# Kernel optimization log

Hardware: AMD Instinct MI355X
Metric: run time of the kernel (lower is better)

Reference implementation:

```python
import jax, jax.numpy as jnp
from jax import lax
import numpy as np

EPS = 1e-5
SCALE, K_UP = 2, 5  # CARAFE defaults


def conv(x, w, pad=0):
    return lax.conv_general_dilated(x, w, (1, 1), [(pad, pad), (pad, pad)],
                                    dimension_numbers=('NCHW', 'OIHW', 'NCHW'))


def bn(x, g, b, m, v):
    # eval-mode BatchNorm2d
    inv = g * lax.rsqrt(v + EPS)
    return x * inv[None, :, None, None] + (b - m * inv)[None, :, None, None]


def carafe(X, comp_w, comp_g, comp_bt, comp_m, comp_v, enc_w, enc_g, enc_bt, enc_m, enc_v):
    b, c, h, w = X.shape
    k2 = K_UP * K_UP
    W = jax.nn.relu(bn(conv(X, comp_w), comp_g, comp_bt, comp_m, comp_v))  # (b, c_mid, h, w)
    W = bn(conv(W, enc_w, pad=1), enc_g, enc_bt, enc_m, enc_v)             # (b, k2*SCALE^2, h, w)
    # PixelShuffle(SCALE): (b, k2*r^2, h, w) -> (b, k2, h*r, w*r)
    W = W.reshape(b, k2, SCALE, SCALE, h, w).transpose(0, 1, 4, 2, 5, 3)
    W = W.reshape(b, k2, h * SCALE, w * SCALE)
    W = jax.nn.softmax(W, axis=1)
    # nearest upsample by SCALE
    Xu = jnp.repeat(jnp.repeat(X, SCALE, axis=2), SCALE, axis=3)
    pad = (K_UP // 2) * SCALE
    Xp = jnp.pad(Xu, ((0, 0), (0, 0), (pad, pad), (pad, pad)))
    h_, w_ = h * SCALE, w * SCALE
    # Unfold(kernel=K_UP, dilation=SCALE): channel-major then kernel index, matching torch
    patches = jnp.stack([Xp[:, :, i * SCALE:i * SCALE + h_, j * SCALE:j * SCALE + w_]
                         for i in range(K_UP) for j in range(K_UP)], axis=2)  # (b,c,k2,h_,w_)
    return jnp.einsum('bkhw,bckhw->bchw', W, patches)


def setup_inputs():
    key = jax.random.key(0)
    ks = iter(jax.random.split(key, 80))
    nk = lambda: next(ks)
    P = lambda shape, s=0.05: jax.random.normal(nk(), shape, jnp.float32) * s
    d = {}
    B, C_out = 4, 64
    cins = [128, 256, 512]
    hw = [(96, 160), (48, 80), (24, 40)]
    for i, (ci, (h, w)) in enumerate(zip(cins, hw)):
        d[f'x{i}'] = jax.random.normal(nk(), (B, ci, h, w), jnp.float32)
        d[f'lat{i}_w'] = P((C_out, ci, 1, 1))
        d[f'lat{i}_b'] = P((C_out,))
        d[f'fpn{i}_w'] = P((C_out, C_out, 3, 3))
        d[f'fpn{i}_b'] = P((C_out,))
    k2s2 = (SCALE * K_UP) ** 2
    for u in range(2):
        d[f'u{u}_comp_w'] = P((C_out, C_out, 1, 1))
        d[f'u{u}_enc_w'] = P((k2s2, C_out, 3, 3))
        for nm, c in [('comp', C_out), ('enc', k2s2)]:
            d[f'u{u}_{nm}_g'] = 1.0 + P((c,))
            d[f'u{u}_{nm}_bt'] = P((c,))
            d[f'u{u}_{nm}_m'] = P((c,))
            d[f'u{u}_{nm}_v'] = jax.random.uniform(nk(), (c,), jnp.float32, 0.5, 1.5)
    return d


def reference(x0, x1, x2,
              lat0_w, lat0_b, fpn0_w, fpn0_b,
              lat1_w, lat1_b, fpn1_w, fpn1_b,
              lat2_w, lat2_b, fpn2_w, fpn2_b,
              u0_comp_w, u0_enc_w, u0_comp_g, u0_comp_bt, u0_comp_m, u0_comp_v,
              u0_enc_g, u0_enc_bt, u0_enc_m, u0_enc_v,
              u1_comp_w, u1_enc_w, u1_comp_g, u1_comp_bt, u1_comp_m, u1_comp_v,
              u1_enc_g, u1_enc_bt, u1_enc_m, u1_enc_v):
    lat = [conv(x, w) + b[None, :, None, None] for x, w, b in
           [(x0, lat0_w, lat0_b), (x1, lat1_w, lat1_b), (x2, lat2_w, lat2_b)]]
    # top-down pathway with CARAFE upsampling
    lat[1] = lat[1] + carafe(lat[2], u1_comp_w, u1_comp_g, u1_comp_bt, u1_comp_m, u1_comp_v,
                             u1_enc_w, u1_enc_g, u1_enc_bt, u1_enc_m, u1_enc_v)
    lat[0] = lat[0] + carafe(lat[1], u0_comp_w, u0_comp_g, u0_comp_bt, u0_comp_m, u0_comp_v,
                             u0_enc_w, u0_enc_g, u0_enc_bt, u0_enc_m, u0_enc_v)
    outs = tuple(conv(l, w, pad=1) + b[None, :, None, None] for l, w, b in
                 [(lat[0], fpn0_w, fpn0_b), (lat[1], fpn1_w, fpn1_b), (lat[2], fpn2_w, fpn2_b)])
    return outs
```

## Files before the change

### kernel.cpp

```cpp
#include <hip/hip_runtime.h>

#define BN_EPS 1e-5f

typedef __attribute__((ext_vector_type(8))) short bf16x8;
typedef __attribute__((ext_vector_type(4))) float f32x4;

__device__ __forceinline__ unsigned short f2bf(float f) {
    unsigned u = __float_as_uint(f);
    return (unsigned short)((u + 0x7fffu + ((u >> 16) & 1u)) >> 16);
}
__device__ __forceinline__ unsigned packbf(float lo, float hi) {
    return ((unsigned)f2bf(hi) << 16) | (unsigned)f2bf(lo);
}
__device__ __forceinline__ float bf2f(unsigned short u) {
    return __uint_as_float((unsigned)u << 16);
}
__device__ __forceinline__ bf16x8 ldw8(const float* p) {
    float4 a = *(const float4*)p;
    float4 b = *(const float4*)(p + 4);
    union { unsigned u[4]; bf16x8 v; } r;
    r.u[0] = packbf(a.x, a.y);
    r.u[1] = packbf(a.z, a.w);
    r.u[2] = packbf(b.x, b.y);
    r.u[3] = packbf(b.z, b.w);
    return r.v;
}

template<int COP, int CSPLIT, int MODE, bool OBF16>
__device__ __forceinline__
void conv3x3_body(int rem, int TX, unsigned short* xs,
                  const unsigned* __restrict__ xp,
                  const unsigned short* __restrict__ wt,
                  const float* __restrict__ p0, const float* __restrict__ p1,
                  const float* __restrict__ p2, const float* __restrict__ p3,
                  float* __restrict__ out, unsigned short* __restrict__ out_us,
                  int H, int W, int C_out)
{
    constexpr int NP = 324;
    constexpr int CT = COP / 16;
    static_assert(CT == CSPLIT, "CPB must be 1 (R1/R2 VGPR cliff)");

    int cs = rem % CSPLIT;
    int b  = (rem / CSPLIT) & 3;
    int t  = rem / (CSPLIT * 4);
    int x0 = (t % TX) * 16, y0 = (t / TX) * 16;

    int tid  = threadIdx.x;
    int lane = tid & 63, wid = tid >> 6;
    int lrow = lane >> 4, lcol = lane & 15;
    int HWp = H * W;

    int co0 = cs * 16;
    bool colok = (x0 + lcol) < W;

    f32x4 accA[2], accB[2];
#pragma unroll
    for (int rr = 0; rr < 2; ++rr) {
        accA[rr] = (f32x4){0.f, 0.f, 0.f, 0.f};
        accB[rr] = (f32x4){0.f, 0.f, 0.f, 0.f};
    }

    unsigned int* wsl = (unsigned int*)xs;

#pragma unroll 1
    for (int kb = 0; kb < 2; ++kb) {
        if (kb) __syncthreads();
        for (int p = tid; p < NP; p += 256) {
            int py = p / 18, px = p - py * 18;
            int gy = y0 + py - 1, gx = x0 + px - 1;
            bool ok = (gy >= 0) && (gy < H) && (gx >= 0) && (gx < W);
            const unsigned* gpp = xp + ((size_t)b * 32 + kb * 16) * HWp
                                     + (size_t)gy * W + gx;
#pragma unroll 8
            for (int cp = 0; cp < 16; ++cp) {
                unsigned pk = ok ? gpp[(size_t)cp * HWp] : 0u;
                wsl[((cp >> 2) * NP + p) * 4 + (cp & 3)] = pk;
            }
        }
        __syncthreads();

        bf16x8 a[9];
        const unsigned short* wl = wt + ((size_t)co0 + lcol) * 64 + kb * 32 + lrow * 8;
#pragma unroll
        for (int t9 = 0; t9 < 9; ++t9)
            a[t9] = *(const bf16x8*)(wl + (size_t)t9 * COP * 64);

#pragma unroll
        for (int rr = 0; rr < 2; ++rr) {
            int r0 = wid + rr * 8;
#pragma unroll
            for (int t9 = 0; t9 < 9; ++t9) {
                int dy = t9 / 3, dx = t9 - dy * 3;
                int g0 = lrow * NP + (r0 + dy) * 18 + lcol + dx;
                bf16x8 b0 = *(const bf16x8*)(xs + (size_t)g0 * 8);
                accA[rr] = __builtin_amdgcn_mfma_f32_16x16x32_bf16(a[t9], b0, accA[rr], 0, 0, 0);
                bf16x8 b1 = *(const bf16x8*)(xs + ((size_t)g0 + 4 * 18) * 8);
                accB[rr] = __builtin_amdgcn_mfma_f32_16x16x32_bf16(a[t9], b1, accB[rr], 0, 0, 0);
            }
        }
    }

    float sc[4], sh[4];
#pragma unroll
    for (int rg = 0; rg < 4; ++rg) {
        int co = co0 + lrow * 4 + rg;
        int cc = (co < C_out) ? co : 0;
        if (MODE == 0) { sc[rg] = 1.f; sh[rg] = p0[cc]; }
        else {
            float inv = p0[cc] * rsqrtf(p3[cc] + BN_EPS);
            sc[rg] = inv; sh[rg] = p1[cc] - p2[cc] * inv;
        }
    }
#pragma unroll
    for (int rr = 0; rr < 2; ++rr) {
        int r0 = wid + rr * 8;
        int yA = y0 + r0, yB = y0 + r0 + 4;
#pragma unroll
        for (int rg = 0; rg < 4; ++rg) {
            int co = co0 + lrow * 4 + rg;
            if (colok && co < C_out) {
                float vA = accA[rr][rg] * sc[rg] + sh[rg];
                float vB = accB[rr][rg] * sc[rg] + sh[rg];
                if (OBF16) {
                    unsigned short* oc = out_us + (((size_t)b * C_out + co) * H) * W + x0 + lcol;
                    if (yA < H) oc[(size_t)yA * W] = f2bf(vA);
                    if (yB < H) oc[(size_t)yB * W] = f2bf(vB);
                } else {
                    float* oc = out + (((size_t)b * C_out + co) * H) * W + x0 + lcol;
                    if (yA < H) oc[(size_t)yA * W] = vA;
                    if (yB < H) oc[(size_t)yB * W] = vB;
                }
            }
        }
    }
}

__global__ __launch_bounds__(256, 6)
void enc_fpn(int encBlocks,
             const unsigned* __restrict__ cxp, const unsigned short* __restrict__ wt_e,
             const float* __restrict__ g, const float* __restrict__ bt,
             const float* __restrict__ m, const float* __restrict__ v,
             unsigned short* __restrict__ enc_us, int He, int We, int TXe,
             const unsigned* __restrict__ xp, const unsigned short* __restrict__ wt_f,
             const float* __restrict__ bias, float* __restrict__ fout,
             int Hf, int Wf, int TXf)
{
    __shared__ unsigned short xs[4 * 324 * 8];
    int f = blockIdx.x;
    if (f < encBlocks)
        conv3x3_body<112, 7, 1, true>(f, TXe, xs, cxp, wt_e,
                                      g, bt, m, v, nullptr, enc_us, He, We, 100);
    else
        conv3x3_body<64, 4, 0, false>(f - encBlocks, TXf, xs, xp, wt_f,
                                      bias, nullptr, nullptr, nullptr, fout, nullptr, Hf, Wf, 64);
}

__global__ __launch_bounds__(256, 6)
void fpn_multi(const unsigned* __restrict__ l0p, const unsigned short* __restrict__ wt0,
               const float* __restrict__ b0, float* __restrict__ o0)
{
    __shared__ unsigned short xs[4 * 324 * 8];
    conv3x3_body<64, 4, 0, false>(blockIdx.x, 10, xs, l0p, wt0,
                                  b0, nullptr, nullptr, nullptr, o0, nullptr, 96, 160, 64);
}

template<int C_IN, int NPX, int MODE, bool INPK>
__device__ __forceinline__
void conv1x1_body(int f, unsigned short* xs,
                  const float* __restrict__ x, const unsigned* __restrict__ xp,
                  const float* __restrict__ wf,
                  const float* __restrict__ p0, const float* __restrict__ p1,
                  const float* __restrict__ p2, const float* __restrict__ p3,
                  unsigned* __restrict__ outp, int HW)
{
    constexpr int NT = NPX / 16;
    constexpr int QUADS = NPX / 4;
    int nb = HW / NPX;
    int px0 = (f % nb) * NPX;
    int b   = f / nb;

    int tid = threadIdx.x;
    int lane = tid & 63, wid = tid >> 6;
    int lrow = lane >> 4, lcol = lane & 15;
    const float*    xb  = INPK ? nullptr : x + (size_t)b * C_IN * HW + px0;
    const unsigned* xpb = INPK ? xp + (size_t)b * (C_IN / 2) * HW + px0 : nullptr;

    f32x4 acc[NT];
#pragma unroll
    for (int nt = 0; nt < NT; ++nt) acc[nt] = (f32x4){0.f, 0.f, 0.f, 0.f};

    for (int cc = 0; cc < C_IN; cc += 32) {
        if (cc) __syncthreads();
        for (int j = tid; j < 16 * QUADS; j += 256) {
            int q  = j & (QUADS - 1);
            int cp = j / QUADS;
            int px = q * 4;
            unsigned* wv = (unsigned*)xs + ((size_t)(cp >> 2) * NPX + px) * 4 + (cp & 3);
            if (INPK) {
                uint4 v = *(const uint4*)(xpb + (size_t)(cc / 2 + cp) * HW + px);
                wv[0] = v.x; wv[4] = v.y; wv[8] = v.z; wv[12] = v.w;
            } else {
                const float* s0 = xb + (size_t)(cc + 2 * cp) * HW + px;
                float4 v0 = *(const float4*)s0;
                float4 v1 = *(const float4*)(s0 + HW);
                wv[0]  = packbf(v0.x, v1.x);
                wv[4]  = packbf(v0.y, v1.y);
                wv[8]  = packbf(v0.z, v1.z);
                wv[12] = packbf(v0.w, v1.w);
            }
        }
        __syncthreads();

        bf16x8 a = ldw8(wf + (size_t)(wid * 16 + lcol) * C_IN + cc + lrow * 8);
#pragma unroll
        for (int nt = 0; nt < NT; ++nt) {
            bf16x8 bf = *(const bf16x8*)(xs + ((size_t)lrow * NPX + nt * 16 + lcol) * 8);
            acc[nt] = __builtin_amdgcn_mfma_f32_16x16x32_bf16(a, bf, acc[nt], 0, 0, 0);
        }
    }

#pragma unroll
    for (int rg = 0; rg < 4; rg += 2) {
        int co = wid * 16 + lrow * 4 + rg;
        float s0, h0, s1, h1;
        if (MODE == 0) { s0 = 1.f; h0 = p0[co]; s1 = 1.f; h1 = p0[co + 1]; }
        else {
            s0 = p0[co] * rsqrtf(p3[co] + BN_EPS);
            h0 = p1[co] - p2[co] * s0;
            s1 = p0[co + 1] * rsqrtf(p3[co + 1] + BN_EPS);
            h1 = p1[co + 1] - p2[co + 1] * s1;
        }
        unsigned* pp = outp + ((size_t)(b * 32 + (co >> 1))) * HW + px0;
#pragma unroll
        for (int nt = 0; nt < NT; ++nt) {
            float r0 = acc[nt][rg] * s0 + h0;
            float r1 = acc[nt][rg + 1] * s1 + h1;
            if (MODE == 1) { r0 = fmaxf(r0, 0.f); r1 = fmaxf(r1, 0.f); }
            pp[nt * 16 + lcol] = packbf(r0, r1);
        }
    }
}

template<int C_IN, int NPX, int MODE, bool INPK>
__global__ __launch_bounds__(256, 4)
void conv1x1_mfma(const float* __restrict__ x, const unsigned* __restrict__ xp,
                  const float* __restrict__ wf,
                  const float* __restrict__ p0, const float* __restrict__ p1,
                  const float* __restrict__ p2, const float* __restrict__ p3,
                  unsigned* __restrict__ outp, int HW)
{
    __shared__ __align__(16) unsigned short xs[4 * NPX * 8];
    int nb = HW / NPX;
    int f = blockIdx.x + nb * blockIdx.z;
    conv1x1_body<C_IN, NPX, MODE, INPK>(f, xs, x, xp, wf, p0, p1, p2, p3, outp, HW);
}

__global__ __launch_bounds__(256, 4)
void lat_prep(const float* __restrict__ x0, const float* __restrict__ w0,
              const float* __restrict__ b0, unsigned* __restrict__ lat0b,
              const float* __restrict__ x1, const float* __restrict__ w1,
              const float* __restrict__ b1, unsigned* __restrict__ lat1b,
              const float* __restrict__ x2, const float* __restrict__ w2,
              const float* __restrict__ b2, unsigned* __restrict__ lat2p,
              const float* __restrict__ f0w, const float* __restrict__ f1w,
              const float* __restrict__ f2w, const float* __restrict__ e0w,
              const float* __restrict__ e1w, unsigned short* __restrict__ wtb)
{
    __shared__ __align__(16) unsigned short xs[4 * 128 * 8];
    int f = blockIdx.x;
    if (f < 480)
        conv1x1_body<128, 128, 0, false>(f, xs, x0, nullptr, w0,
            b0, nullptr, nullptr, nullptr, lat0b, 15360);
    else if (f < 600)
        conv1x1_body<256, 128, 0, false>(f - 480, xs, x1, nullptr, w1,
            b1, nullptr, nullptr, nullptr, lat1b, 3840);
    else if (f < 660)
        conv1x1_body<512, 64, 0, false>(f - 600, xs, x2, nullptr, w2,
            b2, nullptr, nullptr, nullptr, lat2p, 960);
    else {
        int base = (f - 660) * 1024 + threadIdx.x;
#pragma unroll
        for (int t = 0; t < 4; ++t) {
            int i = base + t * 256;
            float v;
            if (i < 110592) {
                int z = i / 36864;
                int rem = i - z * 36864;
                int tap = rem / 4096;
                int r2 = rem - tap * 4096;
                int co = r2 >> 6, ci = r2 & 63;
                const float* src = (z == 0) ? f0w : (z == 1 ? f1w : f2w);
                v = src[((size_t)co * 64 + ci) * 9 + tap];
            } else {
                int j = i - 110592;
                int z = j / 64512;
                int rem = j - z * 64512;
                int tap = rem / 7168;
                int r2 = rem - tap * 7168;
                int co = r2 >> 6, ci = r2 & 63;
                const float* src = z ? e1w : e0w;
                v = (co < 100) ? src[((size_t)co * 64 + ci) * 9 + tap] : 0.f;
            }
            wtb[i] = f2bf(v);
        }
    }
}

template<int CGS>
__global__ __launch_bounds__(256, 4)
void carafe_kernel(const unsigned* __restrict__ srcp,
                   const unsigned short* __restrict__ logits_us,
                   const unsigned* __restrict__ basep, unsigned* __restrict__ dstp,
                   int h, int w)
{
    constexpr int SW = 12, NPX = 144;
    constexpr int CH = 64 / CGS;
    constexpr int CP = CH / 2;
    constexpr int CS = CH + 4;
    __shared__ float ls[NPX * CS];

    int tid = threadIdx.x;
    int x0 = blockIdx.x * 16, y0 = blockIdx.y * 16;
    int b  = blockIdx.z / CGS;
    int cs = blockIdx.z % CGS;
    int H = 2 * h, W = 2 * w;
    int xs0 = (x0 >> 1) - 2, ys0 = (y0 >> 1) - 2;
    size_t hw = (size_t)h * w;
    const unsigned* sb = srcp + ((size_t)(b * 32 + cs * CP)) * hw;

    for (int i = tid; i < NPX * CP; i += 256) {
        int cpl = i / NPX, p = i - cpl * NPX;
        int yy = p / SW, xx = p - yy * SW;
        int sy = ys0 + yy, sx = xs0 + xx;
        unsigned u = 0;
        if (sy >= 0 && sy < h && sx >= 0 && sx < w)
            u = sb[(size_t)cpl * hw + (size_t)sy * w + sx];
        ls[p * CS + 2 * cpl]     = __uint_as_float(u << 16);
        ls[p * CS + 2 * cpl + 1] = __uint_as_float(u & 0xffff0000u);
    }
    __syncthreads();

    int lx = tid & 15, ty = tid >> 4;
    int x = x0 + lx, y = y0 + ty;
    int xw = x >> 1, yh = y >> 1;
    int par = (y & 1) * 2 + (x & 1);

    const unsigned short* lp = logits_us + ((size_t)(b * 100 + par) * h + yh) * w + xw;
    float l[25];
    float mx = -1e30f;
#pragma unroll
    for (int k = 0; k < 25; ++k) {
        l[k] = bf2f(lp[(size_t)(4 * k) * hw]);
        mx = fmaxf(mx, l[k]);
    }
    float s = 0.f;
#pragma unroll
    for (int k = 0; k < 25; ++k) {
        l[k] = __expf(l[k] - mx);
        s += l[k];
    }
    float invs = 1.f / s;
#pragma unroll
    for (int k = 0; k < 25; ++k) l[k] *= invs;

    int pb = (yh - ys0 - 2) * SW + (xw - xs0 - 2);

#pragma unroll 1
    for (int cg = 0; cg < CH / 16; ++cg) {
        float acc[16];
#pragma unroll
        for (int c = 0; c < 16; ++c) acc[c] = 0.f;
#pragma unroll
        for (int k = 0; k < 25; ++k) {
            int ti = k / 5, tj = k - ti * 5;
            const float* q = &ls[(pb + ti * SW + tj) * CS + cg * 16];
            float wk = l[k];
#pragma unroll
            for (int c = 0; c < 16; ++c)
                acc[c] = fmaf(wk, q[c], acc[c]);
        }
        int cbase = cs * CH + cg * 16;
        size_t poff = (((size_t)(b * 32 + (cbase >> 1))) * H + y) * W + x;
        const unsigned* bp = basep + poff;
        unsigned* pp = dstp + poff;
#pragma unroll
        for (int c = 0; c < 16; c += 2) {
            unsigned ub = bp[(size_t)(c >> 1) * H * W];
            float n0 = __uint_as_float(ub << 16) + acc[c];
            float n1 = __uint_as_float(ub & 0xffff0000u) + acc[c + 1];
            pp[(size_t)(c >> 1) * H * W] = packbf(n0, n1);
        }
    }
}

extern "C" void kernel_launch(void* const* d_in, const int* in_sizes, int n_in,
                              void* d_out, int out_size, void* d_ws, size_t ws_size,
                              hipStream_t stream)
{
    const float* x0      = (const float*)d_in[0];
    const float* lat0_w  = (const float*)d_in[1];
    const float* lat0_b  = (const float*)d_in[2];
    const float* fpn0_w  = (const float*)d_in[3];
    const float* fpn0_b  = (const float*)d_in[4];
    const float* x1      = (const float*)d_in[5];
    const float* lat1_w  = (const float*)d_in[6];
    const float* lat1_b  = (const float*)d_in[7];
    const float* fpn1_w  = (const float*)d_in[8];
    const float* fpn1_b  = (const float*)d_in[9];
    const float* x2      = (const float*)d_in[10];
    const float* lat2_w  = (const float*)d_in[11];
    const float* lat2_b  = (const float*)d_in[12];
    const float* fpn2_w  = (const float*)d_in[13];
    const float* fpn2_b  = (const float*)d_in[14];
    const float* u0_comp_w = (const float*)d_in[15];
    const float* u0_enc_w  = (const float*)d_in[16];
    const float* u0_comp_g  = (const float*)d_in[17];
    const float* u0_comp_bt = (const float*)d_in[18];
    const float* u0_comp_m  = (const float*)d_in[19];
    const float* u0_comp_v  = (const float*)d_in[20];
    const float* u0_enc_g   = (const float*)d_in[21];
    const float* u0_enc_bt  = (const float*)d_in[22];
    const float* u0_enc_m   = (const float*)d_in[23];
    const float* u0_enc_v   = (const float*)d_in[24];
    const float* u1_comp_w = (const float*)d_in[25];
    const float* u1_enc_w  = (const float*)d_in[26];
    const float* u1_comp_g  = (const float*)d_in[27];
    const float* u1_comp_bt = (const float*)d_in[28];
    const float* u1_comp_m  = (const float*)d_in[29];
    const float* u1_comp_v  = (const float*)d_in[30];
    const float* u1_enc_g   = (const float*)d_in[31];
    const float* u1_enc_bt  = (const float*)d_in[32];
    const float* u1_enc_m   = (const float*)d_in[33];
    const float* u1_enc_v   = (const float*)d_in[34];

    float* out = (float*)d_out;
    const size_t OUT0 = 4ull * 64 * 96 * 160;
    const size_t OUT1 = 4ull * 64 * 48 * 80;
    const size_t OUT2 = 4ull * 64 * 24 * 40;
    float* out0 = out;
    float* out1 = out + OUT0;
    float* out2 = out + OUT0 + OUT1;

    unsigned* lat0b = (unsigned*)d_ws;
    unsigned* lat1b = lat0b + 1966080;
    unsigned short* wtb = (unsigned short*)(lat1b + 491520);
    unsigned short* wt_fpn0 = wtb;
    unsigned short* wt_fpn1 = wtb + 36864;
    unsigned short* wt_fpn2 = wtb + 73728;
    unsigned short* wt_enc0 = wtb + 110592;
    unsigned short* wt_enc1 = wtb + 175104;
    unsigned* lat0p = (unsigned*)(wtb + 239616);
    unsigned* lat1p = lat0p + 1966080;
    unsigned* lat2p = lat1p + 491520;
    unsigned* compp = lat2p + 122880;
    unsigned short* enc_us = (unsigned short*)(out0 + OUT1);

    dim3 blk(256);

    lat_prep<<<dim3(894), blk, 0, stream>>>(
        x0, lat0_w, lat0_b, lat0b,
        x1, lat1_w, lat1_b, lat1b,
        x2, lat2_w, lat2_b, lat2p,
        fpn0_w, fpn1_w, fpn2_w, u0_enc_w, u1_enc_w, wtb);

    conv1x1_mfma<64, 32, 1, true><<<dim3(30, 1, 4), blk, 0, stream>>>(
        nullptr, lat2p, u1_comp_w, u1_comp_g, u1_comp_bt, u1_comp_m, u1_comp_v,
        compp, 24 * 40);
    enc_fpn<<<dim3(264), blk, 0, stream>>>(168,
        compp, wt_enc1, u1_enc_g, u1_enc_bt, u1_enc_m, u1_enc_v, enc_us, 24, 40, 3,
        lat2p, wt_fpn2, fpn2_b, out2, 24, 40, 3);
    carafe_kernel<2><<<dim3(5, 3, 8), blk, 0, stream>>>(lat2p, enc_us, lat1b, lat1p, 24, 40);

    conv1x1_mfma<64, 32, 1, true><<<dim3(120, 1, 4), blk, 0, stream>>>(
        nullptr, lat1p, u0_comp_w, u0_comp_g, u0_comp_bt, u0_comp_m, u0_comp_v,
        compp, 48 * 80);
    enc_fpn<<<dim3(660), blk, 0, stream>>>(420,
        compp, wt_enc0, u0_enc_g, u0_enc_bt, u0_enc_m, u0_enc_v, enc_us, 48, 80, 5,
        lat1p, wt_fpn1, fpn1_b, out1, 48, 80, 5);
    carafe_kernel<2><<<dim3(10, 6, 8), blk, 0, stream>>>(lat1p, enc_us, lat0b, lat0p, 48, 80);

    fpn_multi<<<dim3(960), blk, 0, stream>>>(lat0p, wt_fpn0, fpn0_b, out0);
}
```

Before: 272.4 us.

## Switch intermediate bf16 activations and encoder logits to channel-last layout

Intermediate packed-bf16 feature maps change from channel-planar to pixel-major layout, with 32 packed channel pairs contiguous per pixel. The encoder logits change the same way, with 100 channels contiguous per pixel. The conv3x3 and conv1x1 staging loops, the CARAFE source and base loads, and the output stores now use 16-byte vector accesses instead of strided scalar ones, cutting memory transactions across several kernels. The encoder's bf16 output is now written as scattered 2-byte stores at a 200-byte pixel stride, which may coalesce worse. The host-side producers and consumers not shown must agree with the new layout.

```diff
diff --git a/kernel.cpp b/kernel.cpp
--- a/kernel.cpp
+++ b/kernel.cpp
@@ -26,6 +26,7 @@
     return r.v;
 }
 
+
 template<int COP, int CSPLIT, int MODE, bool OBF16>
 __device__ __forceinline__
 void conv3x3_body(int rem, int TX, unsigned short* xs,
@@ -61,21 +62,19 @@
     }
 
     unsigned int* wsl = (unsigned int*)xs;
+    const unsigned* xb = xp + (size_t)b * HWp * 32;
 
 #pragma unroll 1
     for (int kb = 0; kb < 2; ++kb) {
         if (kb) __syncthreads();
-        for (int p = tid; p < NP; p += 256) {
+        for (int it = tid; it < NP * 4; it += 256) {
+            int p = it >> 2, g = it & 3;
             int py = p / 18, px = p - py * 18;
             int gy = y0 + py - 1, gx = x0 + px - 1;
-            bool ok = (gy >= 0) && (gy < H) && (gx >= 0) && (gx < W);
-            const unsigned* gpp = xp + ((size_t)b * 32 + kb * 16) * HWp
-                                     + (size_t)gy * W + gx;
-#pragma unroll 8
-            for (int cp = 0; cp < 16; ++cp) {
-                unsigned pk = ok ? gpp[(size_t)cp * HWp] : 0u;
-                wsl[((cp >> 2) * NP + p) * 4 + (cp & 3)] = pk;
-            }
+            uint4 v = make_uint4(0u, 0u, 0u, 0u);
+            if (gy >= 0 && gy < H && gx >= 0 && gx < W)
+                v = *(const uint4*)(xb + ((size_t)gy * W + gx) * 32 + kb * 16 + g * 4);
+            *(uint4*)(wsl + ((size_t)g * NP + p) * 4) = v;
         }
         __syncthreads();
 
@@ -115,20 +114,33 @@
     for (int rr = 0; rr < 2; ++rr) {
         int r0 = wid + rr * 8;
         int yA = y0 + r0, yB = y0 + r0 + 4;
-#pragma unroll
-        for (int rg = 0; rg < 4; ++rg) {
-            int co = co0 + lrow * 4 + rg;
-            if (colok && co < C_out) {
-                float vA = accA[rr][rg] * sc[rg] + sh[rg];
-                float vB = accB[rr][rg] * sc[rg] + sh[rg];
-                if (OBF16) {
-                    unsigned short* oc = out_us + (((size_t)b * C_out + co) * H) * W + x0 + lcol;
-                    if (yA < H) oc[(size_t)yA * W] = f2bf(vA);
-                    if (yB < H) oc[(size_t)yB * W] = f2bf(vB);
-                } else {
+        if (OBF16) {
+            if (colok) {
+                if (yA < H) {
+                    unsigned short* oc = out_us + (((size_t)b * H + yA) * W + x0 + lcol) * 100;
+#pragma unroll
+                    for (int rg = 0; rg < 4; ++rg) {
+                        int co = co0 + lrow * 4 + rg;
+                        if (co < C_out) oc[co] = f2bf(accA[rr][rg] * sc[rg] + sh[rg]);
+                    }
+                }
+                if (yB < H) {
+                    unsigned short* oc = out_us + (((size_t)b * H + yB) * W + x0 + lcol) * 100;
+#pragma unroll
+                    for (int rg = 0; rg < 4; ++rg) {
+                        int co = co0 + lrow * 4 + rg;
+                        if (co < C_out) oc[co] = f2bf(accB[rr][rg] * sc[rg] + sh[rg]);
+                    }
+                }
+            }
+        } else {
+#pragma unroll
+            for (int rg = 0; rg < 4; ++rg) {
+                int co = co0 + lrow * 4 + rg;
+                if (colok && co < C_out) {
                     float* oc = out + (((size_t)b * C_out + co) * H) * W + x0 + lcol;
-                    if (yA < H) oc[(size_t)yA * W] = vA;
-                    if (yB < H) oc[(size_t)yB * W] = vB;
+                    if (yA < H) oc[(size_t)yA * W] = accA[rr][rg] * sc[rg] + sh[rg];
+                    if (yB < H) oc[(size_t)yB * W] = accB[rr][rg] * sc[rg] + sh[rg];
                 }
             }
         }
@@ -183,7 +195,7 @@
     int lane = tid & 63, wid = tid >> 6;
     int lrow = lane >> 4, lcol = lane & 15;
     const float*    xb  = INPK ? nullptr : x + (size_t)b * C_IN * HW + px0;
-    const unsigned* xpb = INPK ? xp + (size_t)b * (C_IN / 2) * HW + px0 : nullptr;
+    const unsigned* xpb = INPK ? xp + ((size_t)b * HW + px0) * 32 : nullptr;
 
     f32x4 acc[NT];
 #pragma unroll
@@ -191,18 +203,21 @@
 
     for (int cc = 0; cc < C_IN; cc += 32) {
         if (cc) __syncthreads();
-        for (int j = tid; j < 16 * QUADS; j += 256) {
-            int q  = j & (QUADS - 1);
-            int cp = j / QUADS;
-            int px = q * 4;
-            unsigned* wv = (unsigned*)xs + ((size_t)(cp >> 2) * NPX + px) * 4 + (cp & 3);
-            if (INPK) {
-                uint4 v = *(const uint4*)(xpb + (size_t)(cc / 2 + cp) * HW + px);
-                wv[0] = v.x; wv[4] = v.y; wv[8] = v.z; wv[12] = v.w;
-            } else {
+        if (INPK) {
+            for (int it = tid; it < NPX * 4; it += 256) {
+                int px = it >> 2, g = it & 3;
+                uint4 v = *(const uint4*)(xpb + (size_t)px * 32 + cc / 2 + g * 4);
+                *(uint4*)((unsigned*)xs + ((size_t)g * NPX + px) * 4) = v;
+            }
+        } else {
+            for (int j = tid; j < 16 * QUADS; j += 256) {
+                int q  = j & (QUADS - 1);
+                int cp = j / QUADS;
+                int px = q * 4;
                 const float* s0 = xb + (size_t)(cc + 2 * cp) * HW + px;
                 float4 v0 = *(const float4*)s0;
                 float4 v1 = *(const float4*)(s0 + HW);
+                unsigned* wv = (unsigned*)xs + ((size_t)(cp >> 2) * NPX + px) * 4 + (cp & 3);
                 wv[0]  = packbf(v0.x, v1.x);
                 wv[4]  = packbf(v0.y, v1.y);
                 wv[8]  = packbf(v0.z, v1.z);
@@ -219,25 +234,27 @@
         }
     }
 
-#pragma unroll
-    for (int rg = 0; rg < 4; rg += 2) {
+    float sc[4], sh[4];
+#pragma unroll
+    for (int rg = 0; rg < 4; ++rg) {
         int co = wid * 16 + lrow * 4 + rg;
-        float s0, h0, s1, h1;
-        if (MODE == 0) { s0 = 1.f; h0 = p0[co]; s1 = 1.f; h1 = p0[co + 1]; }
+        if (MODE == 0) { sc[rg] = 1.f; sh[rg] = p0[co]; }
         else {
-            s0 = p0[co] * rsqrtf(p3[co] + BN_EPS);
-            h0 = p1[co] - p2[co] * s0;
-            s1 = p0[co + 1] * rsqrtf(p3[co + 1] + BN_EPS);
-            h1 = p1[co + 1] - p2[co + 1] * s1;
-        }
-        unsigned* pp = outp + ((size_t)(b * 32 + (co >> 1))) * HW + px0;
-#pragma unroll
-        for (int nt = 0; nt < NT; ++nt) {
-            float r0 = acc[nt][rg] * s0 + h0;
-            float r1 = acc[nt][rg + 1] * s1 + h1;
-            if (MODE == 1) { r0 = fmaxf(r0, 0.f); r1 = fmaxf(r1, 0.f); }
-            pp[nt * 16 + lcol] = packbf(r0, r1);
-        }
+            float inv = p0[co] * rsqrtf(p3[co] + BN_EPS);
+            sc[rg] = inv; sh[rg] = p1[co] - p2[co] * inv;
+        }
+    }
+    unsigned* pp = outp + ((size_t)b * HW + px0) * 32 + wid * 8 + lrow * 2;
+#pragma unroll
+    for (int nt = 0; nt < NT; ++nt) {
+        float r[4];
+#pragma unroll
+        for (int rg = 0; rg < 4; ++rg) {
+            r[rg] = acc[nt][rg] * sc[rg] + sh[rg];
+            if (MODE == 1) r[rg] = fmaxf(r[rg], 0.f);
+        }
+        uint2 pk = make_uint2(packbf(r[0], r[1]), packbf(r[2], r[3]));
+        *(uint2*)(pp + (size_t)(nt * 16 + lcol) * 32) = pk;
     }
 }
 
@@ -315,7 +332,6 @@
 {
     constexpr int SW = 12, NPX = 144;
     constexpr int CH = 64 / CGS;
-    constexpr int CP = CH / 2;
     constexpr int CS = CH + 4;
     __shared__ float ls[NPX * CS];
 
@@ -326,17 +342,20 @@
     int H = 2 * h, W = 2 * w;
     int xs0 = (x0 >> 1) - 2, ys0 = (y0 >> 1) - 2;
     size_t hw = (size_t)h * w;
-    const unsigned* sb = srcp + ((size_t)(b * 32 + cs * CP)) * hw;
-
-    for (int i = tid; i < NPX * CP; i += 256) {
-        int cpl = i / NPX, p = i - cpl * NPX;
+    const unsigned* sb = srcp + (size_t)b * hw * 32 + cs * 16;
+
+    for (int i = tid; i < NPX * 4; i += 256) {
+        int p = i >> 2, g = i & 3;
         int yy = p / SW, xx = p - yy * SW;
         int sy = ys0 + yy, sx = xs0 + xx;
-        unsigned u = 0;
+        uint4 u = make_uint4(0u, 0u, 0u, 0u);
         if (sy >= 0 && sy < h && sx >= 0 && sx < w)
-            u = sb[(size_t)cpl * hw + (size_t)sy * w + sx];
-        ls[p * CS + 2 * cpl]     = __uint_as_float(u << 16);
-        ls[p * CS + 2 * cpl + 1] = __uint_as_float(u & 0xffff0000u);
+            u = *(const uint4*)(sb + ((size_t)sy * w + sx) * 32 + g * 4);
+        float* lq = &ls[p * CS + g * 8];
+        lq[0] = __uint_as_float(u.x << 16); lq[1] = __uint_as_float(u.x & 0xffff0000u);
+        lq[2] = __uint_as_float(u.y << 16); lq[3] = __uint_as_float(u.y & 0xffff0000u);
+        lq[4] = __uint_as_float(u.z << 16); lq[5] = __uint_as_float(u.z & 0xffff0000u);
+        lq[6] = __uint_as_float(u.w << 16); lq[7] = __uint_as_float(u.w & 0xffff0000u);
     }
     __syncthreads();
 
@@ -345,12 +364,12 @@
     int xw = x >> 1, yh = y >> 1;
     int par = (y & 1) * 2 + (x & 1);
 
-    const unsigned short* lp = logits_us + ((size_t)(b * 100 + par) * h + yh) * w + xw;
+    const unsigned short* lp = logits_us + ((size_t)b * hw + (size_t)yh * w + xw) * 100 + par;
     float l[25];
     float mx = -1e30f;
 #pragma unroll
     for (int k = 0; k < 25; ++k) {
-        l[k] = bf2f(lp[(size_t)(4 * k) * hw]);
+        l[k] = bf2f(lp[4 * k]);
         mx = fmaxf(mx, l[k]);
     }
     float s = 0.f;
@@ -379,17 +398,19 @@
             for (int c = 0; c < 16; ++c)
                 acc[c] = fmaf(wk, q[c], acc[c]);
         }
-        int cbase = cs * CH + cg * 16;
-        size_t poff = (((size_t)(b * 32 + (cbase >> 1))) * H + y) * W + x;
-        const unsigned* bp = basep + poff;
-        unsigned* pp = dstp + poff;
-#pragma unroll
-        for (int c = 0; c < 16; c += 2) {
-            unsigned ub = bp[(size_t)(c >> 1) * H * W];
-            float n0 = __uint_as_float(ub << 16) + acc[c];
-            float n1 = __uint_as_float(ub & 0xffff0000u) + acc[c + 1];
-            pp[(size_t)(c >> 1) * H * W] = packbf(n0, n1);
-        }
+        size_t poff = (((size_t)b * H + y) * W + x) * 32 + cs * 16 + cg * 8;
+        uint4 ba = *(const uint4*)(basep + poff);
+        uint4 bb = *(const uint4*)(basep + poff + 4);
+        unsigned bu[8] = {ba.x, ba.y, ba.z, ba.w, bb.x, bb.y, bb.z, bb.w};
+        unsigned ou[8];
+#pragma unroll
+        for (int j = 0; j < 8; ++j) {
+            float n0 = __uint_as_float(bu[j] << 16) + acc[2 * j];
+            float n1 = __uint_as_float(bu[j] & 0xffff0000u) + acc[2 * j + 1];
+            ou[j] = packbf(n0, n1);
+        }
+        *(uint4*)(dstp + poff)     = make_uint4(ou[0], ou[1], ou[2], ou[3]);
+        *(uint4*)(dstp + poff + 4) = make_uint4(ou[4], ou[5], ou[6], ou[7]);
     }
 }
 
```

Result: faster. 248.7 us (-8.7%).
